# Optimization experiments

Hardware: AMD Instinct MI355X
Metric: run time of the kernel (lower is better)

Reference implementation:

```python
import jax, jax.numpy as jnp
import numpy as np

NX, NY = 512, 512  # n_pillars_x, n_pillars_y
B, N_POINTS, C = 4, 100000, 64


def setup_inputs() -> dict:
    key = jax.random.key(0)
    kx, ki = jax.random.split(key)
    x = jax.random.normal(kx, (B, N_POINTS, C), dtype=jnp.float32)
    indices = jax.random.randint(ki, (B, N_POINTS), 0, NX * NY, dtype=jnp.int64)
    return {"x": x, "indices": indices}


def reference(x, indices):
    # scatter-add point features into dense pillar grid: (B, P, C)
    P = NX * NY
    scatter = lambda xb, ib: jax.ops.segment_sum(xb, ib, num_segments=P)
    grid = jax.vmap(scatter)(x, indices)            # (B, P, C)
    grid = jnp.transpose(grid, (0, 2, 1))           # (B, C, P)
    grid = grid.reshape(x.shape[0], x.shape[2], NX, NY)  # (B, C, NX, NY)
    return grid
```

## Files before the change

kernel.cpp:

```cpp
#include <hip/hip_runtime.h>

#define PFN_NX     512
#define PFN_NY     512
#define PFN_P      (PFN_NX * PFN_NY)
#define PFN_B      4
#define PFN_NPTS   100000
#define PFN_C      64
#define PFN_NBIN   (PFN_B * PFN_P)
#define PFN_TOTPTS (PFN_B * PFN_NPTS)


__global__ __launch_bounds__(256) void pfn_hist(const int* __restrict__ idx,
                                                int* __restrict__ counts) {
    int pi = blockIdx.x * 256 + threadIdx.x;
    if (pi >= PFN_TOTPTS) return;
    int b = (unsigned)pi / PFN_NPTS;
    atomicAdd(&counts[b * PFN_P + idx[pi]], 1);
}

__global__ __launch_bounds__(256) void pfn_block_reduce(const int4* __restrict__ counts4,
                                                        int* __restrict__ partials) {
    __shared__ int s[256];
    int t = threadIdx.x, g = blockIdx.x;
    int4 v = counts4[g * 256 + t];
    s[t] = v.x + v.y + v.z + v.w;
    __syncthreads();
    for (int off = 128; off > 0; off >>= 1) {
        if (t < off) s[t] += s[t + off];
        __syncthreads();
    }
    if (t == 0) partials[g] = s[0];
}

__global__ __launch_bounds__(256) void pfn_scan(const int4* __restrict__ counts4,
                                                const int*  __restrict__ partials,
                                                int* __restrict__ offsets) {
    __shared__ int s[256];
    __shared__ int base_sh;
    const int t = threadIdx.x, g = blockIdx.x;

    int4 pv = ((const int4*)partials)[t];
    int psum = pv.x + pv.y + pv.z + pv.w;
    s[t] = psum;
    __syncthreads();
    for (int off = 1; off < 256; off <<= 1) {
        int add = (t >= off) ? s[t - off] : 0;
        __syncthreads();
        s[t] += add;
        __syncthreads();
    }
    const int q = g >> 2, r = g & 3;
    if (t == q) {
        int excl = s[q] - psum;
        if (r > 0) excl += pv.x;
        if (r > 1) excl += pv.y;
        if (r > 2) excl += pv.z;
        base_sh = excl;
    }
    if (g == 0 && t == 255) offsets[PFN_NBIN] = s[255];
    __syncthreads();
    const int base = base_sh;
    __syncthreads();

    int4 v = counts4[g * 256 + t];
    int sum = v.x + v.y + v.z + v.w;
    s[t] = sum;
    __syncthreads();
    for (int off = 1; off < 256; off <<= 1) {
        int add = (t >= off) ? s[t - off] : 0;
        __syncthreads();
        s[t] += add;
        __syncthreads();
    }
    int excl = s[t] - sum + base;
    int4 o;
    o.x = excl;
    o.y = excl + v.x;
    o.z = excl + v.x + v.y;
    o.w = excl + v.x + v.y + v.z;
    ((int4*)offsets)[g * 256 + t] = o;
}

__global__ __launch_bounds__(256) void pfn_reorder(const int* __restrict__ idx,
                                                   const int* __restrict__ offsets,
                                                   int* __restrict__ counts,
                                                   int* __restrict__ order) {
    int pi = blockIdx.x * 256 + threadIdx.x;
    if (pi >= PFN_TOTPTS) return;
    int b = (unsigned)pi / PFN_NPTS;
    int bp = b * PFN_P + idx[pi];
    int old = atomicSub(&counts[bp], 1);
    order[offsets[bp] + old - 1] = pi;
}

__global__ __launch_bounds__(256) void pfn_gather(const float* __restrict__ x,
                                                  const int*   __restrict__ offsets,
                                                  const int*   __restrict__ order,
                                                  float*       __restrict__ out) {
    __shared__ float tile[64][65];
    const int g    = blockIdx.x;
    const int bp0  = g << 6;
    const int b    = bp0 >> 18;
    const int p0   = bp0 & (PFN_P - 1);
    const int wave = threadIdx.x >> 6;
    const int lane = threadIdx.x & 63;
    const int wb0  = bp0 + wave * 16;

    int off_l = 0;
    if (lane <= 16) off_l = offsets[wb0 + lane];
    const int o_base = __shfl(off_l, 0);
    const int o_end  = __shfl(off_l, 16);
    const int cnt    = o_end - o_base;

    if (cnt <= 64) {
#pragma unroll
        for (int k = 0; k < 16; ++k) tile[lane][wave * 16 + k] = 0.f;

        int ord_l = (lane < cnt) ? order[o_base + lane] : 0;

        int myBin = 0;
#pragma unroll
        for (int j = 1; j < 16; ++j)
            myBin += ((__shfl(off_l, j) - o_base) <= lane) ? 1 : 0;

        for (int b0 = 0; b0 < cnt; b0 += 8) {
            float pre[8];
            int   col[8];
#pragma unroll
            for (int k = 0; k < 8; ++k) {
                const int t = b0 + k;
                if (t < cnt) {
                    const int pi = __shfl(ord_l, t);
                    col[k] = wave * 16 + __shfl(myBin, t);
                    pre[k] = x[((size_t)pi << 6) + lane];
                }
            }
#pragma unroll
            for (int k = 0; k < 8; ++k) {
                const int t = b0 + k;
                if (t < cnt) tile[lane][col[k]] += pre[k];
            }
        }
    } else {
        for (int j = 0; j < 16; ++j) {
            const int start = __shfl(off_l, j);
            const int end   = __shfl(off_l, j + 1);
            float s = 0.f;
            for (int t = start; t < end; ++t) {
                const int pi = order[t];
                s += x[((size_t)pi << 6) + lane];
            }
            tile[lane][wave * 16 + j] = s;
        }
    }
    __syncthreads();

    const size_t outBase = (size_t)b << 24;
#pragma unroll
    for (int k = 0; k < 4; ++k) {
        const int id = k * 256 + threadIdx.x;
        const int c  = id >> 4;
        const int i  = id & 15;
        float4 v;
        v.x = tile[c][4 * i + 0];
        v.y = tile[c][4 * i + 1];
        v.z = tile[c][4 * i + 2];
        v.w = tile[c][4 * i + 3];
        *(float4*)(out + outBase + ((size_t)c << 18) + p0 + 4 * i) = v;
    }
}

extern "C" void kernel_launch(void* const* d_in, const int* in_sizes, int n_in,
                              void* d_out, int out_size, void* d_ws, size_t ws_size,
                              hipStream_t stream) {
    const float* x   = (const float*)d_in[0];
    const int*   idx = (const int*)  d_in[1];
    float*       out = (float*)d_out;

    int* counts   = (int*)d_ws;
    int* offsets  = counts + PFN_NBIN;
    int* partials = offsets + PFN_NBIN + 1;
    int* order    = partials + 1024;

    hipMemsetAsync(counts, 0, (size_t)PFN_NBIN * sizeof(int), stream);
    pfn_hist<<<(PFN_TOTPTS + 255) / 256, 256, 0, stream>>>(idx, counts);
    pfn_block_reduce<<<1024, 256, 0, stream>>>((const int4*)counts, partials);
    pfn_scan<<<1024, 256, 0, stream>>>((const int4*)counts, partials, offsets);
    pfn_reorder<<<(PFN_TOTPTS + 255) / 256, 256, 0, stream>>>(idx, offsets, counts, order);
    pfn_gather<<<PFN_NBIN / 64, 256, 0, stream>>>(x, offsets, order, out);
}
```

Measured before the change: 391.0 us.

## Replace counting-sort bucketing with atomicExch linked lists per pillar

Instead of a histogram, two-level scan and reorder pass, each point is pushed onto a per-bin linked list with atomicExch, and the gather kernel walks the lists for 16 bins per wave in lockstep. This removes three kernel launches and the scan traffic, at the cost of a serial dependent load chain per bin in the gather and nondeterministic summation order. Output stores also switch to nontemporal vector stores to avoid polluting cache with the large dense grid.

After: 360.4 us. 7.8% less time.

```diff
diff --git a/kernel.cpp b/kernel.cpp
--- a/kernel.cpp
+++ b/kernel.cpp
@@ -9,93 +9,22 @@
 #define PFN_NBIN   (PFN_B * PFN_P)
 #define PFN_TOTPTS (PFN_B * PFN_NPTS)
 
+typedef float f32x4 __attribute__((ext_vector_type(4)));
 
-__global__ __launch_bounds__(256) void pfn_hist(const int* __restrict__ idx,
-                                                int* __restrict__ counts) {
+
+__global__ __launch_bounds__(256) void pfn_build(const int* __restrict__ idx,
+                                                 int* __restrict__ head,
+                                                 int* __restrict__ nxt) {
     int pi = blockIdx.x * 256 + threadIdx.x;
     if (pi >= PFN_TOTPTS) return;
-    int b = (unsigned)pi / PFN_NPTS;
-    atomicAdd(&counts[b * PFN_P + idx[pi]], 1);
-}
-
-__global__ __launch_bounds__(256) void pfn_block_reduce(const int4* __restrict__ counts4,
-                                                        int* __restrict__ partials) {
-    __shared__ int s[256];
-    int t = threadIdx.x, g = blockIdx.x;
-    int4 v = counts4[g * 256 + t];
-    s[t] = v.x + v.y + v.z + v.w;
-    __syncthreads();
-    for (int off = 128; off > 0; off >>= 1) {
-        if (t < off) s[t] += s[t + off];
-        __syncthreads();
-    }
-    if (t == 0) partials[g] = s[0];
-}
-
-__global__ __launch_bounds__(256) void pfn_scan(const int4* __restrict__ counts4,
-                                                const int*  __restrict__ partials,
-                                                int* __restrict__ offsets) {
-    __shared__ int s[256];
-    __shared__ int base_sh;
-    const int t = threadIdx.x, g = blockIdx.x;
-
-    int4 pv = ((const int4*)partials)[t];
-    int psum = pv.x + pv.y + pv.z + pv.w;
-    s[t] = psum;
-    __syncthreads();
-    for (int off = 1; off < 256; off <<= 1) {
-        int add = (t >= off) ? s[t - off] : 0;
-        __syncthreads();
-        s[t] += add;
-        __syncthreads();
-    }
-    const int q = g >> 2, r = g & 3;
-    if (t == q) {
-        int excl = s[q] - psum;
-        if (r > 0) excl += pv.x;
-        if (r > 1) excl += pv.y;
-        if (r > 2) excl += pv.z;
-        base_sh = excl;
-    }
-    if (g == 0 && t == 255) offsets[PFN_NBIN] = s[255];
-    __syncthreads();
-    const int base = base_sh;
-    __syncthreads();
-
-    int4 v = counts4[g * 256 + t];
-    int sum = v.x + v.y + v.z + v.w;
-    s[t] = sum;
-    __syncthreads();
-    for (int off = 1; off < 256; off <<= 1) {
-        int add = (t >= off) ? s[t - off] : 0;
-        __syncthreads();
-        s[t] += add;
-        __syncthreads();
-    }
-    int excl = s[t] - sum + base;
-    int4 o;
-    o.x = excl;
-    o.y = excl + v.x;
-    o.z = excl + v.x + v.y;
-    o.w = excl + v.x + v.y + v.z;
-    ((int4*)offsets)[g * 256 + t] = o;
-}
-
-__global__ __launch_bounds__(256) void pfn_reorder(const int* __restrict__ idx,
-                                                   const int* __restrict__ offsets,
-                                                   int* __restrict__ counts,
-                                                   int* __restrict__ order) {
-    int pi = blockIdx.x * 256 + threadIdx.x;
-    if (pi >= PFN_TOTPTS) return;
-    int b = (unsigned)pi / PFN_NPTS;
+    int b  = (unsigned)pi / PFN_NPTS;
     int bp = b * PFN_P + idx[pi];
-    int old = atomicSub(&counts[bp], 1);
-    order[offsets[bp] + old - 1] = pi;
+    nxt[pi] = atomicExch(&head[bp], pi);
 }
 
 __global__ __launch_bounds__(256) void pfn_gather(const float* __restrict__ x,
-                                                  const int*   __restrict__ offsets,
-                                                  const int*   __restrict__ order,
+                                                  const int*   __restrict__ head,
+                                                  const int*   __restrict__ nxt,
                                                   float*       __restrict__ out) {
     __shared__ float tile[64][65];
     const int g    = blockIdx.x;
@@ -106,52 +35,30 @@
     const int lane = threadIdx.x & 63;
     const int wb0  = bp0 + wave * 16;
 
-    int off_l = 0;
-    if (lane <= 16) off_l = offsets[wb0 + lane];
-    const int o_base = __shfl(off_l, 0);
-    const int o_end  = __shfl(off_l, 16);
-    const int cnt    = o_end - o_base;
+    int cur = -1;
+    if (lane < 16) cur = head[wb0 + lane];
 
-    if (cnt <= 64) {
 #pragma unroll
-        for (int k = 0; k < 16; ++k) tile[lane][wave * 16 + k] = 0.f;
+    for (int k = 0; k < 16; ++k) tile[lane][wave * 16 + k] = 0.f;
 
-        int ord_l = (lane < cnt) ? order[o_base + lane] : 0;
+    unsigned long long m;
+    while ((m = __ballot(cur >= 0)) != 0ull) {
+        int nxtv = -1;
+        if (cur >= 0) nxtv = nxt[cur];
 
-        int myBin = 0;
+        float pre[16];
 #pragma unroll
-        for (int j = 1; j < 16; ++j)
-            myBin += ((__shfl(off_l, j) - o_base) <= lane) ? 1 : 0;
-
-        for (int b0 = 0; b0 < cnt; b0 += 8) {
-            float pre[8];
-            int   col[8];
-#pragma unroll
-            for (int k = 0; k < 8; ++k) {
-                const int t = b0 + k;
-                if (t < cnt) {
-                    const int pi = __shfl(ord_l, t);
-                    col[k] = wave * 16 + __shfl(myBin, t);
-                    pre[k] = x[((size_t)pi << 6) + lane];
-                }
-            }
-#pragma unroll
-            for (int k = 0; k < 8; ++k) {
-                const int t = b0 + k;
-                if (t < cnt) tile[lane][col[k]] += pre[k];
+        for (int j = 0; j < 16; ++j) {
+            if ((m >> j) & 1ull) {
+                const int pi = __shfl(cur, j);
+                pre[j] = x[((size_t)pi << 6) + lane];
             }
         }
-    } else {
+#pragma unroll
         for (int j = 0; j < 16; ++j) {
-            const int start = __shfl(off_l, j);
-            const int end   = __shfl(off_l, j + 1);
-            float s = 0.f;
-            for (int t = start; t < end; ++t) {
-                const int pi = order[t];
-                s += x[((size_t)pi << 6) + lane];
-            }
-            tile[lane][wave * 16 + j] = s;
+            if ((m >> j) & 1ull) tile[lane][wave * 16 + j] += pre[j];
         }
+        cur = nxtv;
     }
     __syncthreads();
 
@@ -161,12 +68,13 @@
         const int id = k * 256 + threadIdx.x;
         const int c  = id >> 4;
         const int i  = id & 15;
-        float4 v;
+        f32x4 v;
         v.x = tile[c][4 * i + 0];
         v.y = tile[c][4 * i + 1];
         v.z = tile[c][4 * i + 2];
         v.w = tile[c][4 * i + 3];
-        *(float4*)(out + outBase + ((size_t)c << 18) + p0 + 4 * i) = v;
+        __builtin_nontemporal_store(
+            v, (f32x4*)(out + outBase + ((size_t)c << 18) + p0 + 4 * i));
     }
 }
 
@@ -177,15 +85,10 @@
     const int*   idx = (const int*)  d_in[1];
     float*       out = (float*)d_out;
 
-    int* counts   = (int*)d_ws;
-    int* offsets  = counts + PFN_NBIN;
-    int* partials = offsets + PFN_NBIN + 1;
-    int* order    = partials + 1024;
+    int* head = (int*)d_ws;
+    int* nxt  = head + PFN_NBIN;
 
-    hipMemsetAsync(counts, 0, (size_t)PFN_NBIN * sizeof(int), stream);
-    pfn_hist<<<(PFN_TOTPTS + 255) / 256, 256, 0, stream>>>(idx, counts);
-    pfn_block_reduce<<<1024, 256, 0, stream>>>((const int4*)counts, partials);
-    pfn_scan<<<1024, 256, 0, stream>>>((const int4*)counts, partials, offsets);
-    pfn_reorder<<<(PFN_TOTPTS + 255) / 256, 256, 0, stream>>>(idx, offsets, counts, order);
-    pfn_gather<<<PFN_NBIN / 64, 256, 0, stream>>>(x, offsets, order, out);
+    (void)hipMemsetAsync(head, 0xFF, (size_t)PFN_NBIN * sizeof(int), stream);
+    pfn_build<<<(PFN_TOTPTS + 255) / 256, 256, 0, stream>>>(idx, head, nxt);
+    pfn_gather<<<PFN_NBIN / 64, 256, 0, stream>>>(x, head, nxt, out);
 }
```
